# Optimization experiments

Measured on AMD Instinct MI355X. Metric: run time of the kernel, lower is better.

Reference implementation:

```python
import jax, jax.numpy as jnp
import numpy as np

N_CLASSES = 3  # hardcoded in the original module (labels == 0/1/2)
EPS = 1e-12    # F.normalize default eps


def setup_inputs() -> dict:
    key = jax.random.key(0)
    k1, k2, k3 = jax.random.split(key, 3)
    query = jax.random.normal(k1, (32768, 256), dtype=jnp.float32)
    memory = jax.random.normal(k2, (3, 512, 256), dtype=jnp.float32)
    labels = jax.random.randint(k3, (32768,), 0, 3, dtype=jnp.int64)
    return {"query": query, "labels": labels, "memory": memory}


def reference(query, labels, memory):
    C, n_cells, d = memory.shape  # (3, 512, 256)
    # ---- read: cross-attention over all C*n_cells memory slots ----
    mem_flat = memory.reshape(C * n_cells, d)
    scores = jax.nn.softmax(query @ mem_flat.T, axis=1)  # (N, C*n_cells)
    q_read = scores @ mem_flat                           # (N, d) == the per-row loop, batched

    # ---- update (training path): masked softmax over queries per class ----
    def upd(c):
        mask = labels == c                               # (N,)
        logits = query @ memory[c].T                     # (N, n_cells)
        logits = jnp.where(mask[:, None], logits, -jnp.inf)
        sq = jax.nn.softmax(logits, axis=0)              # softmax over (masked) queries
        delta = sq.T @ query                             # (n_cells, d); zero rows contribute 0
        new = memory[c] + delta
        norm = jnp.maximum(jnp.linalg.norm(new, axis=1, keepdims=True), EPS)
        return new / norm                                # F.normalize over dim=1

    new_mem = jnp.stack([upd(c) for c in range(C)])      # C is a small fixed constant (3)
    return q_read, jax.lax.stop_gradient(new_mem)        # original detaches updated memory
```

## Files before the change

### kernel.cpp

```cpp
#include <hip/hip_runtime.h>
#include <math.h>

#define NQ    32768
#define DDIM  256
#define NCLS  3
#define CELLS 512
#define STOT  1536
#define BK    32

typedef __attribute__((ext_vector_type(8)))  short bf16x8;
typedef __attribute__((ext_vector_type(16))) float f32x16;

#define ROWF(r) (((r) & 3) + 8 * ((r) >> 2) + 4 * lh)

__device__ __forceinline__ f32x16 mfma16(bf16x8 a, bf16x8 b, f32x16 c) {
    return __builtin_amdgcn_mfma_f32_32x32x16_bf16(a, b, c, 0, 0, 0);
}
__device__ __forceinline__ unsigned short f2bf(float f) {
    const unsigned u = __float_as_uint(f);
    return (unsigned short)((u + 0x7FFFu + ((u >> 16) & 1u)) >> 16);
}
__device__ __forceinline__ float bf2f(unsigned short b) {
    return __uint_as_float(((unsigned)b) << 16);
}
__device__ __forceinline__ void gl16(const unsigned short* g, unsigned short* l) {
    __builtin_amdgcn_global_load_lds(
        (const __attribute__((address_space(1))) unsigned int*)g,
        (__attribute__((address_space(3))) unsigned int*)l, 16, 0, 0);
}

__global__ __launch_bounds__(256) void k_convert(const float* __restrict__ src,
        unsigned short* __restrict__ hi, unsigned short* __restrict__ lo,
        unsigned short* __restrict__ hiT, float* __restrict__ sq, int R) {
    __shared__ unsigned short lh_s[64][65];
    const int r0 = blockIdx.x * 64, k0 = blockIdx.y * 64, t = threadIdx.x;
#pragma unroll
    for (int it = 0; it < 4; ++it) {
        const int idx = t + 256 * it;
        const int rl = idx >> 4, kq = idx & 15;
        const float4 v = *(const float4*)(src + (size_t)(r0 + rl) * DDIM + k0 + kq * 4);
        const unsigned short h0 = f2bf(v.x), h1 = f2bf(v.y), h2 = f2bf(v.z), h3 = f2bf(v.w);
        const unsigned short l0 = f2bf(v.x - bf2f(h0)), l1 = f2bf(v.y - bf2f(h1));
        const unsigned short l2 = f2bf(v.z - bf2f(h2)), l3 = f2bf(v.w - bf2f(h3));
        ushort4 hv; hv.x = h0; hv.y = h1; hv.z = h2; hv.w = h3;
        ushort4 lv; lv.x = l0; lv.y = l1; lv.z = l2; lv.w = l3;
        *(ushort4*)(hi + (size_t)(r0 + rl) * DDIM + k0 + kq * 4) = hv;
        *(ushort4*)(lo + (size_t)(r0 + rl) * DDIM + k0 + kq * 4) = lv;
        lh_s[rl][kq * 4 + 0] = h0; lh_s[rl][kq * 4 + 1] = h1;
        lh_s[rl][kq * 4 + 2] = h2; lh_s[rl][kq * 4 + 3] = h3;
        float ssq = v.x * v.x + v.y * v.y + v.z * v.z + v.w * v.w;
        ssq += __shfl_xor(ssq, 1, 64);
        ssq += __shfl_xor(ssq, 2, 64);
        ssq += __shfl_xor(ssq, 4, 64);
        ssq += __shfl_xor(ssq, 8, 64);
        if (kq == 0) atomicAdd(&sq[r0 + rl], ssq);
    }
    __syncthreads();
#pragma unroll
    for (int it = 0; it < 16; ++it) {
        const int idx = t + 256 * it;
        const int kl = idx >> 6, rl = idx & 63;
        hiT[(size_t)(k0 + kl) * R + r0 + rl] = lh_s[rl][kl];
    }
}

__global__ __launch_bounds__(256) void k_pe(
        const unsigned short* __restrict__ Qhi, const unsigned short* __restrict__ Qlo,
        const unsigned short* __restrict__ Mhi, const unsigned short* __restrict__ Mlo,
        const int* __restrict__ labels, const float* __restrict__ qn2,
        const float* __restrict__ mn2,
        unsigned short* __restrict__ P, unsigned short* __restrict__ ET,
        int ibase, int ch, int ipg) {
    __shared__ unsigned short smem[2][2][2][128][BK];
    typedef unsigned short trt[32][40];
    trt* trP = (trt*)&smem[0][0][0][0][0];
    trt* trE = trP + 4;

    const int t = threadIdx.x, lane = t & 63, wid = t >> 6;
    const int l31 = lane & 31, lh = lane >> 5;
    const int wi = wid >> 1, wj = wid & 1;
    int ib, jb;
    if (ipg > 0) {
        const int xcd = blockIdx.x & 7, s = blockIdx.x >> 3;
        jb = s % 12; ib = xcd * ipg + s / 12;
    } else { jb = blockIdx.x % 12; ib = blockIdx.x / 12; }
    const int iblk = ib * 128, jblk = jb * 128;
    const int iloc0 = iblk + wi * 64;
    const int j0    = jblk + wj * 64;
    const int cblk  = jb >> 2;

    const int c0 = wid * 128 + lane, c1 = c0 + 64;
    const int r0 = c0 >> 2, o0 = ((c0 ^ (c0 >> 3)) & 3) * 8;
    const int r1 = c1 >> 2, o1 = ((c1 ^ (c1 >> 3)) & 3) * 8;
    const unsigned short* gA[2] = { Qhi + (size_t)(ibase + iblk) * DDIM,
                                    Qlo + (size_t)(ibase + iblk) * DDIM };
    const unsigned short* gB[2] = { Mhi + (size_t)jblk * DDIM,
                                    Mlo + (size_t)jblk * DDIM };
    auto STAGE = [&](int b, int k0) {
#pragma unroll
        for (int h = 0; h < 2; ++h) {
            gl16(gA[h] + (size_t)r0 * DDIM + k0 + o0, &smem[b][0][h][0][0] + c0 * 8);
            gl16(gA[h] + (size_t)r1 * DDIM + k0 + o1, &smem[b][0][h][0][0] + c1 * 8);
            gl16(gB[h] + (size_t)r0 * DDIM + k0 + o0, &smem[b][1][h][0][0] + c0 * 8);
            gl16(gB[h] + (size_t)r1 * DDIM + k0 + o1, &smem[b][1][h][0][0] + c1 * 8);
        }
    };

    f32x16 acc[2][2] = {};
    const int ra0 = wi * 64 + l31, ra1 = ra0 + 32;
    const int rb0 = wj * 64 + l31, rb1 = rb0 + 32;
    const int swa = (ra0 >> 1) & 3;
    const int swb = (rb0 >> 1) & 3;
    STAGE(0, 0);
    for (int s = 0; s < DDIM / BK; ++s) {
        __syncthreads();
        if (s + 1 < DDIM / BK) STAGE((s + 1) & 1, (s + 1) * BK);
        const int b = s & 1;
#pragma unroll
        for (int t16 = 0; t16 < 2; ++t16) {
            const int oc = t16 * 2 + lh;
            const int ka = (oc ^ swa) * 8, kb = (oc ^ swb) * 8;
            const bf16x8 a0h = *(const bf16x8*)&smem[b][0][0][ra0][ka];
            const bf16x8 a1h = *(const bf16x8*)&smem[b][0][0][ra1][ka];
            const bf16x8 a0l = *(const bf16x8*)&smem[b][0][1][ra0][ka];
            const bf16x8 a1l = *(const bf16x8*)&smem[b][0][1][ra1][ka];
            const bf16x8 b0h = *(const bf16x8*)&smem[b][1][0][rb0][kb];
            const bf16x8 b1h = *(const bf16x8*)&smem[b][1][0][rb1][kb];
            const bf16x8 b0l = *(const bf16x8*)&smem[b][1][1][rb0][kb];
            const bf16x8 b1l = *(const bf16x8*)&smem[b][1][1][rb1][kb];
            acc[0][0] = mfma16(a0h, b0h, acc[0][0]);
            acc[0][0] = mfma16(a0h, b0l, acc[0][0]);
            acc[0][0] = mfma16(a0l, b0h, acc[0][0]);
            acc[0][1] = mfma16(a0h, b1h, acc[0][1]);
            acc[0][1] = mfma16(a0h, b1l, acc[0][1]);
            acc[0][1] = mfma16(a0l, b1h, acc[0][1]);
            acc[1][0] = mfma16(a1h, b0h, acc[1][0]);
            acc[1][0] = mfma16(a1h, b0l, acc[1][0]);
            acc[1][0] = mfma16(a1l, b0h, acc[1][0]);
            acc[1][1] = mfma16(a1h, b1h, acc[1][1]);
            acc[1][1] = mfma16(a1h, b1l, acc[1][1]);
            acc[1][1] = mfma16(a1l, b1h, acc[1][1]);
        }
    }
    __syncthreads();

#pragma unroll
    for (int ti = 0; ti < 2; ++ti) {
        float qn[16]; unsigned lm = 0;
        const int ig0 = ibase + iloc0 + ti * 32;
#pragma unroll
        for (int r = 0; r < 16; ++r) {
            const int ir = ig0 + ROWF(r);
            qn[r] = 6.0f * sqrtf(qn2[ir]);
            lm |= (unsigned)(labels[ir] == cblk) << r;
        }
#pragma unroll
        for (int tj = 0; tj < 2; ++tj) {
            const int jg = j0 + tj * 32 + l31;
            const float mn = 6.0f * sqrtf(mn2[jg]);
#pragma unroll
            for (int r = 0; r < 16; ++r) {
                const float lg = acc[ti][tj][r];
                trP[wid][ROWF(r)][l31] = f2bf(__expf(lg - qn[r]));
                const float e = ((lm >> r) & 1u) ? __expf(lg - mn) : 0.0f;
                trE[wid][l31][ROWF(r)] = f2bf(e);
            }
            const int rr = lane >> 1, off = (lane & 1) * 16;
            {
                const unsigned short* lp = &trP[wid][rr][off];
                const bf16x8 w0 = *(const bf16x8*)(lp);
                const bf16x8 w1 = *(const bf16x8*)(lp + 8);
                unsigned short* prow = P + (size_t)(iloc0 + ti * 32 + rr) * STOT
                                         + j0 + tj * 32 + off;
                *(bf16x8*)(prow)     = w0;
                *(bf16x8*)(prow + 8) = w1;
            }
            {
                const unsigned short* lp = &trE[wid][rr][off];
                const bf16x8 w0 = *(const bf16x8*)(lp);
                const bf16x8 w1 = *(const bf16x8*)(lp + 8);
                unsigned short* erow = ET + (size_t)(j0 + tj * 32 + rr) * ch
                                          + iloc0 + ti * 32 + off;
                *(bf16x8*)(erow)     = w0;
                *(bf16x8*)(erow + 8) = w1;
            }
        }
    }
}

__global__ __launch_bounds__(256) void k_pv(const unsigned short* __restrict__ P,
        const unsigned short* __restrict__ MhiT,
        float* __restrict__ out, int ibase) {
    __shared__ unsigned short sP[2][64][64];
    __shared__ unsigned short sV[2][128][64];
    const int t = threadIdx.x, lane = t & 63, wid = t >> 6;
    const int l31 = lane & 31, lh = lane >> 5;
    const int wq = wid >> 1, wd = wid & 1;
    const int qblk = blockIdx.x * 64, dblk = blockIdx.y * 128;
    const int d0 = dblk + wd * 64;
    const unsigned short* gP = P + (size_t)qblk * STOT;
    const unsigned short* gV = MhiT + (size_t)dblk * STOT;

    auto STAGE = [&](int b, int k0) {
#pragma unroll
        for (int it = 0; it < 2; ++it) {
            const int c = wid * 128 + it * 64 + lane;
            const int r = c >> 3, o = ((c & 7) ^ (r & 7)) * 8;
            gl16(gP + (size_t)r * STOT + k0 + o, &sP[b][0][0] + c * 8);
        }
#pragma unroll
        for (int it = 0; it < 4; ++it) {
            const int c = wid * 256 + it * 64 + lane;
            const int r = c >> 3, o = ((c & 7) ^ (r & 7)) * 8;
            gl16(gV + (size_t)r * STOT + k0 + o, &sV[b][0][0] + c * 8);
        }
    };

    bf16x8 bones;
    const short ob = (l31 == 0) ? (short)0x3F80 : (short)0;
#pragma unroll
    for (int e = 0; e < 8; ++e) bones[e] = ob;

    f32x16 acc[2] = {};
    f32x16 accS = {};
    const int rp = wq * 32 + l31, rv0 = wd * 64 + l31, rv1 = rv0 + 32;
    STAGE(0, 0);
    for (int s = 0; s < STOT / 64; ++s) {
        __syncthreads();
        if (s + 1 < STOT / 64) STAGE((s + 1) & 1, (s + 1) * 64);
        const int b = s & 1;
#pragma unroll
        for (int t16 = 0; t16 < 4; ++t16) {
            const int oc = t16 * 2 + lh;
            const bf16x8 a0 = *(const bf16x8*)&sP[b][rp][(oc ^ (rp & 7)) * 8];
            const bf16x8 b0 = *(const bf16x8*)&sV[b][rv0][(oc ^ (rv0 & 7)) * 8];
            const bf16x8 b1 = *(const bf16x8*)&sV[b][rv1][(oc ^ (rv1 & 7)) * 8];
            acc[0] = mfma16(a0, b0, acc[0]);
            acc[1] = mfma16(a0, b1, acc[1]);
            accS   = mfma16(a0, bones, accS);
        }
    }
    float rinv[16];
#pragma unroll
    for (int r = 0; r < 16; ++r) rinv[r] = 1.f / __shfl(accS[r], lh << 5, 64);
#pragma unroll
    for (int td = 0; td < 2; ++td) {
#pragma unroll
        for (int r = 0; r < 16; ++r) {
            const int ig = ibase + qblk + wq * 32 + ROWF(r);
            out[(size_t)ig * DDIM + d0 + td * 32 + l31] = acc[td][r] * rinv[r];
        }
    }
}

__global__ __launch_bounds__(256) void k_delta4(const unsigned short* __restrict__ ET,
        const unsigned short* __restrict__ QhiT,
        float* __restrict__ delta, float* __restrict__ colsum,
        int ibase, int ch, int ppx) {
    __shared__ unsigned short sE[2][128][64];
    __shared__ unsigned short sQ[2][128][64];
    const int t = threadIdx.x, lane = t & 63, wid = t >> 6;
    const int l31 = lane & 31, lh = lane >> 5;
    const int wj = wid >> 1, wd = wid & 1;
    int jb, db, kb;
    if (ppx > 0) {
        const int xcd = blockIdx.x & 7, s = blockIdx.x >> 3;
        jb = s % 12;
        const int pidx = xcd * ppx + s / 12;
        kb = pidx >> 1; db = pidx & 1;
    } else {
        jb = blockIdx.x % 12; db = (blockIdx.x / 12) & 1; kb = blockIdx.x / 24;
    }
    const int jblk = jb * 128, dblk = db * 128, i0 = kb * 1024;
    const int j0 = jblk + wj * 64, d0 = dblk + wd * 64;
    const unsigned short* gE = ET + (size_t)jblk * ch + i0;
    const unsigned short* gQ = QhiT + (size_t)dblk * NQ + ibase + i0;

    auto STAGE = [&](int b, int k0) {
#pragma unroll
        for (int it = 0; it < 4; ++it) {
            const int c = wid * 256 + it * 64 + lane;
            const int r = c >> 3, o = ((c & 7) ^ (r & 7)) * 8;
            gl16(gE + (size_t)r * ch + k0 + o, &sE[b][0][0] + c * 8);
            gl16(gQ + (size_t)r * NQ + k0 + o, &sQ[b][0][0] + c * 8);
        }
    };

    bf16x8 bones;
    const short ob = (l31 == 0) ? (short)0x3F80 : (short)0;
#pragma unroll
    for (int e = 0; e < 8; ++e) bones[e] = ob;

    f32x16 acc[2][2] = {};
    f32x16 accS0 = {}, accS1 = {};
    const int re0 = wj * 64 + l31, re1 = re0 + 32;
    const int rq0 = wd * 64 + l31, rq1 = rq0 + 32;
    STAGE(0, 0);
    for (int s = 0; s < 16; ++s) {
        __syncthreads();
        if (s + 1 < 16) STAGE((s + 1) & 1, (s + 1) * 64);
        const int b = s & 1;
#pragma unroll
        for (int t16 = 0; t16 < 4; ++t16) {
            const int oc = t16 * 2 + lh;
            const bf16x8 a0 = *(const bf16x8*)&sE[b][re0][(oc ^ (re0 & 7)) * 8];
            const bf16x8 a1 = *(const bf16x8*)&sE[b][re1][(oc ^ (re1 & 7)) * 8];
            const bf16x8 b0 = *(const bf16x8*)&sQ[b][rq0][(oc ^ (rq0 & 7)) * 8];
            const bf16x8 b1 = *(const bf16x8*)&sQ[b][rq1][(oc ^ (rq1 & 7)) * 8];
            acc[0][0] = mfma16(a0, b0, acc[0][0]);
            acc[0][1] = mfma16(a0, b1, acc[0][1]);
            acc[1][0] = mfma16(a1, b0, acc[1][0]);
            acc[1][1] = mfma16(a1, b1, acc[1][1]);
            if (wd == 0) {
                accS0 = mfma16(a0, bones, accS0);
                accS1 = mfma16(a1, bones, accS1);
            }
        }
    }
#pragma unroll
    for (int tj = 0; tj < 2; ++tj) {
#pragma unroll
        for (int td = 0; td < 2; ++td) {
#pragma unroll
            for (int r = 0; r < 16; ++r) {
                const int jr = j0 + tj * 32 + ROWF(r);
                atomicAdd(&delta[(size_t)jr * DDIM + d0 + td * 32 + l31], acc[tj][td][r]);
            }
        }
    }
    if (wd == 0 && l31 == 0) {
#pragma unroll
        for (int r = 0; r < 16; ++r) {
            atomicAdd(&colsum[j0 + ROWF(r)], accS0[r]);
            atomicAdd(&colsum[j0 + 32 + ROWF(r)], accS1[r]);
        }
    }
}

__global__ void k_final(const float* __restrict__ M,
                        const float* __restrict__ delta,
                        const float* __restrict__ colsum,
                        float* __restrict__ out) {
    const int row  = blockIdx.x * 4 + (threadIdx.x >> 6);
    const int lane = threadIdx.x & 63;
    const float inv = 1.f / colsum[row];
    const float4 mv = *(const float4*)(M + (size_t)row * DDIM + lane * 4);
    const float4 dv = *(const float4*)(delta + (size_t)row * DDIM + lane * 4);
    float4 nv;
    nv.x = fmaf(dv.x, inv, mv.x);
    nv.y = fmaf(dv.y, inv, mv.y);
    nv.z = fmaf(dv.z, inv, mv.z);
    nv.w = fmaf(dv.w, inv, mv.w);
    float ss = nv.x * nv.x + nv.y * nv.y + nv.z * nv.z + nv.w * nv.w;
#pragma unroll
    for (int sh = 1; sh < 64; sh <<= 1) ss += __shfl_xor(ss, sh, 64);
    const float rn = 1.f / fmaxf(sqrtf(ss), 1e-12f);
    nv.x *= rn; nv.y *= rn; nv.z *= rn; nv.w *= rn;
    *(float4*)(out + (size_t)NQ * DDIM + (size_t)row * DDIM + lane * 4) = nv;
}

extern "C" void kernel_launch(void* const* d_in, const int* in_sizes, int n_in,
                              void* d_out, int out_size, void* d_ws, size_t ws_size,
                              hipStream_t stream) {
    const float* Q      = (const float*)d_in[0];
    const int*   labels = (const int*)d_in[1];
    const float* M      = (const float*)d_in[2];
    float* out = (float*)d_out;

    char* p = (char*)d_ws;
    float* colsum = (float*)p;          p += (size_t)STOT * 4;
    float* delta  = (float*)p;          p += (size_t)STOT * DDIM * 4;
    float* qn2    = (float*)p;          p += (size_t)NQ * 4;
    float* mn2    = (float*)p;          p += (size_t)STOT * 4;
    const size_t zero_bytes = (size_t)(p - (char*)d_ws);
    unsigned short* Qhi  = (unsigned short*)p; p += (size_t)NQ * DDIM * 2;
    unsigned short* Qlo  = (unsigned short*)p; p += (size_t)NQ * DDIM * 2;
    unsigned short* QhiT = (unsigned short*)p; p += (size_t)NQ * DDIM * 2;
    unsigned short* Mhi  = (unsigned short*)p; p += (size_t)STOT * DDIM * 2;
    unsigned short* Mlo  = (unsigned short*)p; p += (size_t)STOT * DDIM * 2;
    unsigned short* MhiT = (unsigned short*)p; p += (size_t)STOT * DDIM * 2;
    const size_t fixed_bytes = (size_t)(p - (char*)d_ws);

    int nch = 2;
    while (nch < 32 &&
           fixed_bytes + (size_t)(NQ / nch) * STOT * 2 * 2 > ws_size) nch <<= 1;
    const int ch = NQ / nch;
    unsigned short* Pbuf = (unsigned short*)p;
    unsigned short* ETb  = Pbuf + (size_t)ch * STOT;

    const int ipg    = ((ch / 128) % 8 == 0) ? (ch / 128) / 8 : 0;
    const int ksplit = ch / 1024;
    const int ppx    = ((2 * ksplit) % 8 == 0) ? (2 * ksplit) / 8 : 0;

    hipMemsetAsync(d_ws, 0, zero_bytes, stream);

    k_convert<<<dim3(NQ / 64, 4), 256, 0, stream>>>(Q, Qhi, Qlo, QhiT, qn2, NQ);
    k_convert<<<dim3(STOT / 64, 4), 256, 0, stream>>>(M, Mhi, Mlo, MhiT, mn2, STOT);

    for (int h = 0; h < nch; ++h) {
        const int ibase = h * ch;
        k_pe<<<12 * (ch / 128), 256, 0, stream>>>(Qhi, Qlo, Mhi, Mlo, labels,
                                                  qn2, mn2, Pbuf, ETb, ibase, ch, ipg);
        k_pv<<<dim3(ch / 64, 2), 256, 0, stream>>>(Pbuf, MhiT, out, ibase);
        k_delta4<<<24 * ksplit, 256, 0, stream>>>(ETb, QhiT, delta, colsum,
                                                  ibase, ch, ppx);
    }
    k_final<<<STOT / 4, 256, 0, stream>>>(M, delta, colsum, out);
}
```

Before: 303.9 us.

## Prefetch two stages ahead with partial vmcnt waits in GEMM kernels

Restructures the double-buffered main loops of three GEMM kernels so two stages are issued up front. Each iteration waits only until the older stage's direct-to-LDS loads have landed (partial vmcnt) rather than draining every load with __syncthreads. After computing, a barrier guards buffer reuse before the next prefetch is issued. This lets global loads overlap more compute, but the hand-written waitcnt counts must exactly match the loads each thread issues per stage, and getting them wrong would cause races.

Result: faster. 295.9 us (-2.6%).

```diff
diff --git a/kernel.cpp b/kernel.cpp
--- a/kernel.cpp
+++ b/kernel.cpp
@@ -12,6 +12,9 @@
 typedef __attribute__((ext_vector_type(16))) float f32x16;
 
 #define ROWF(r) (((r) & 3) + 8 * ((r) >> 2) + 4 * lh)
+
+#define PIPE_WAIT_BAR(N) asm volatile("s_waitcnt vmcnt(" #N ")\n\ts_barrier" ::: "memory")
+#define PIPE_BAR()       asm volatile("s_barrier" ::: "memory")
 
 __device__ __forceinline__ f32x16 mfma16(bf16x8 a, bf16x8 b, f32x16 c) {
     return __builtin_amdgcn_mfma_f32_32x32x16_bf16(a, b, c, 0, 0, 0);
@@ -111,11 +114,7 @@
     const int rb0 = wj * 64 + l31, rb1 = rb0 + 32;
     const int swa = (ra0 >> 1) & 3;
     const int swb = (rb0 >> 1) & 3;
-    STAGE(0, 0);
-    for (int s = 0; s < DDIM / BK; ++s) {
-        __syncthreads();
-        if (s + 1 < DDIM / BK) STAGE((s + 1) & 1, (s + 1) * BK);
-        const int b = s & 1;
+    auto COMPUTE = [&](int b) {
 #pragma unroll
         for (int t16 = 0; t16 < 2; ++t16) {
             const int oc = t16 * 2 + lh;
@@ -141,7 +140,18 @@
             acc[1][1] = mfma16(a1h, b1l, acc[1][1]);
             acc[1][1] = mfma16(a1l, b1h, acc[1][1]);
         }
-    }
+    };
+
+    STAGE(0, 0);
+    STAGE(1, BK);
+    for (int s = 0; s < DDIM / BK - 1; ++s) {
+        PIPE_WAIT_BAR(8);
+        COMPUTE(s & 1);
+        PIPE_BAR();
+        if (s + 2 < DDIM / BK) STAGE(s & 1, (s + 2) * BK);
+    }
+    PIPE_WAIT_BAR(0);
+    COMPUTE(1);
     __syncthreads();
 
 #pragma unroll
@@ -224,11 +234,7 @@
     f32x16 acc[2] = {};
     f32x16 accS = {};
     const int rp = wq * 32 + l31, rv0 = wd * 64 + l31, rv1 = rv0 + 32;
-    STAGE(0, 0);
-    for (int s = 0; s < STOT / 64; ++s) {
-        __syncthreads();
-        if (s + 1 < STOT / 64) STAGE((s + 1) & 1, (s + 1) * 64);
-        const int b = s & 1;
+    auto COMPUTE = [&](int b) {
 #pragma unroll
         for (int t16 = 0; t16 < 4; ++t16) {
             const int oc = t16 * 2 + lh;
@@ -239,7 +245,19 @@
             acc[1] = mfma16(a0, b1, acc[1]);
             accS   = mfma16(a0, bones, accS);
         }
-    }
+    };
+
+    STAGE(0, 0);
+    STAGE(1, 64);
+    for (int s = 0; s < STOT / 64 - 1; ++s) {
+        PIPE_WAIT_BAR(6);
+        COMPUTE(s & 1);
+        PIPE_BAR();
+        if (s + 2 < STOT / 64) STAGE(s & 1, (s + 2) * 64);
+    }
+    PIPE_WAIT_BAR(0);
+    COMPUTE(1);
+
     float rinv[16];
 #pragma unroll
     for (int r = 0; r < 16; ++r) rinv[r] = 1.f / __shfl(accS[r], lh << 5, 64);
@@ -295,11 +313,7 @@
     f32x16 accS0 = {}, accS1 = {};
     const int re0 = wj * 64 + l31, re1 = re0 + 32;
     const int rq0 = wd * 64 + l31, rq1 = rq0 + 32;
-    STAGE(0, 0);
-    for (int s = 0; s < 16; ++s) {
-        __syncthreads();
-        if (s + 1 < 16) STAGE((s + 1) & 1, (s + 1) * 64);
-        const int b = s & 1;
+    auto COMPUTE = [&](int b) {
 #pragma unroll
         for (int t16 = 0; t16 < 4; ++t16) {
             const int oc = t16 * 2 + lh;
@@ -316,7 +330,19 @@
                 accS1 = mfma16(a1, bones, accS1);
             }
         }
-    }
+    };
+
+    STAGE(0, 0);
+    STAGE(1, 64);
+    for (int s = 0; s < 15; ++s) {
+        PIPE_WAIT_BAR(8);
+        COMPUTE(s & 1);
+        PIPE_BAR();
+        if (s + 2 < 16) STAGE(s & 1, (s + 2) * 64);
+    }
+    PIPE_WAIT_BAR(0);
+    COMPUTE(1);
+
 #pragma unroll
     for (int tj = 0; tj < 2; ++tj) {
 #pragma unroll
```
